# Kernel optimization log

Measured on AMD Instinct MI355X. Metric: run time of the kernel, lower is better.

## Reference

```python
import jax, jax.numpy as jnp
import numpy as np

NQ = 6; DM = 128; CH = 4; SEQ = 2048; CHUNK = 16; BATCH = 128
NFP = 5 * NQ * 2   # feature params for 2 layers
NMP = 5 * NQ * 2   # mixing params for 2 layers

# ---- batched gate matrices (theta: (B,)) ----

def _rx(t):
    c = jnp.cos(t / 2).astype(jnp.complex64)
    s = (-1j * jnp.sin(t / 2)).astype(jnp.complex64)
    return jnp.stack([jnp.stack([c, s], -1), jnp.stack([s, c], -1)], -2)

def _ry(t):
    c = jnp.cos(t / 2).astype(jnp.complex64)
    s = jnp.sin(t / 2).astype(jnp.complex64)
    return jnp.stack([jnp.stack([c, -s], -1), jnp.stack([s, c], -1)], -2)

def _rz(t):
    e = jnp.exp(-1j * t.astype(jnp.complex64) / 2)
    z = jnp.zeros_like(e)
    return jnp.stack([jnp.stack([e, z], -1), jnp.stack([z, jnp.conj(e)], -1)], -2)

def _crx(t):
    B = t.shape[0]
    r = _rx(t)
    I = jnp.broadcast_to(jnp.eye(2, dtype=jnp.complex64), (B, 2, 2))
    Z = jnp.zeros((B, 2, 2), jnp.complex64)
    return jnp.concatenate([jnp.concatenate([I, Z], -1), jnp.concatenate([Z, r], -1)], -2)

# ---- batched statevector gate application; state: (B, 2, ..., 2) with axis 1+w = wire w ----

def _ap1(s, U, w):
    s = jnp.moveaxis(s, 1 + w, 1)
    sh = s.shape
    s = jnp.einsum('bij,bjr->bir', U, s.reshape(sh[0], 2, -1)).reshape(sh)
    return jnp.moveaxis(s, 1, 1 + w)

def _ap2(s, U, w0, w1):
    s = jnp.moveaxis(s, (1 + w0, 1 + w1), (1, 2))
    sh = s.shape
    s = jnp.einsum('bij,bjr->bir', U, s.reshape(sh[0], 4, -1)).reshape(sh)
    return jnp.moveaxis(s, (1, 2), (1 + w0, 1 + w1))

def _ansatz(s, p, off):
    # RX,RY,RZ on each qubit, then forward CRX ring, then backward CRX ring
    for i in range(NQ):
        s = _ap1(s, _rx(p[:, off + 3 * i]), i)
        s = _ap1(s, _ry(p[:, off + 3 * i + 1]), i)
        s = _ap1(s, _rz(p[:, off + 3 * i + 2]), i)
    off += 3 * NQ
    for i in range(NQ):
        s = _ap2(s, _crx(p[:, off]), i, (i + 1) % NQ)
        off += 1
    for i in range(NQ - 1, -1, -1):
        s = _ap2(s, _crx(p[:, off]), i, (i - 1) % NQ)
        off += 1
    return s, off

def _circuit(angles, fp, mp):
    B = angles.shape[0]
    s = jnp.zeros((B, 2 ** NQ), jnp.complex64).at[:, 0].set(1.0).reshape((B,) + (2,) * NQ)
    for i in range(NQ):                      # RY input embedding
        s = _ap1(s, _ry(angles[:, i]), i)
    off = 0
    for _ in range(2):                        # feature layers
        s, off = _ansatz(s, fp, off)
    off = 0
    for _ in range(2):                        # mixing layers
        s, off = _ansatz(s, mp, off)
    xs, ys, zs = [], [], []
    for i in range(NQ):                       # <X_i>, <Y_i>, <Z_i>
        v = jnp.moveaxis(s, 1 + i, 1).reshape(B, 2, -1)
        a, b = v[:, 0], v[:, 1]
        ab = jnp.sum(jnp.conj(a) * b, -1)
        xs.append(2 * jnp.real(ab))
        ys.append(2 * jnp.imag(ab))
        zs.append(jnp.sum(jnp.abs(a) ** 2 - jnp.abs(b) ** 2, -1))
    return jnp.stack(xs + ys + zs, 1)         # (B, 18) ordered X..Y..Z

def _ln(x, g, b, eps=1e-5):
    m = x.mean(-1, keepdims=True)
    v = ((x - m) ** 2).mean(-1, keepdims=True)
    return (x - m) / jnp.sqrt(v + eps) * g + b

def _fwd(x, conv_w, conv_b, ln1_g, ln1_b, ca1_w, ca1_b, ca2_w, ca2_b, pp_w, pp_b,
         ep_w, ep_b, op_w, op_b, ln2_g, ln2_b, sa1_w, sa1_b, sa2_w, sa2_b,
         cl1_w, cl1_b, cl2_w, cl2_b):
    B, C, S = x.shape
    h = jax.lax.conv_general_dilated(x, conv_w, (1,), [(1, 1)],
                                     dimension_numbers=('NCH', 'OIH', 'NCH')) + conv_b[None, :, None]
    h = jnp.transpose(h, (0, 2, 1))           # (B, S, D)
    h = _ln(h, ln1_g, ln1_b)
    nchunks = S // CHUNK
    h = h.reshape(B * nchunks, CHUNK, DM)
    sc = jnp.tanh(h @ ca1_w + ca1_b) @ ca2_w + ca2_b
    w = jax.nn.softmax(sc, axis=1)
    summ = jnp.sum(w * h, axis=1)             # (B*nchunks, D)
    ap = summ @ pp_w + pp_b
    fp, mp = ap[:, :NFP], ap[:, NFP:]
    ang = jnp.tanh(summ @ ep_w + ep_b) * np.pi
    q = _circuit(ang, fp, mp)                 # (B*nchunks, 18)
    cf = jax.nn.silu(_ln(q @ op_w + op_b, ln2_g, ln2_b))  # dropout = eval identity
    cf = cf.reshape(B, nchunks, DM)
    ss = jnp.tanh(cf @ sa1_w + sa1_b) @ sa2_w + sa2_b
    sw = jax.nn.softmax(ss, axis=1)
    rep = jnp.sum(sw * cf, axis=1)
    return jax.nn.silu(rep @ cl1_w + cl1_b) @ cl2_w + cl2_b

def setup_inputs() -> dict:
    key = jax.random.key(0)
    ks = jax.random.split(key, 16)
    n = lambda k, sh: (jax.random.normal(k, sh, jnp.float32) * 0.05)
    return {
        'x': jax.random.normal(ks[0], (BATCH, CH, SEQ), jnp.float32),
        'conv_w': n(ks[1], (DM, CH, 3)), 'conv_b': jnp.zeros((DM,), jnp.float32),
        'ln1_g': jnp.ones((DM,), jnp.float32), 'ln1_b': jnp.zeros((DM,), jnp.float32),
        'ca1_w': n(ks[2], (DM, DM // 4)), 'ca1_b': jnp.zeros((DM // 4,), jnp.float32),
        'ca2_w': n(ks[3], (DM // 4, 1)), 'ca2_b': jnp.zeros((1,), jnp.float32),
        'pp_w': n(ks[4], (DM, NFP + NMP)), 'pp_b': jnp.zeros((NFP + NMP,), jnp.float32),
        'ep_w': n(ks[5], (DM, NQ)), 'ep_b': jnp.zeros((NQ,), jnp.float32),
        'op_w': n(ks[6], (3 * NQ, DM)), 'op_b': jnp.zeros((DM,), jnp.float32),
        'ln2_g': jnp.ones((DM,), jnp.float32), 'ln2_b': jnp.zeros((DM,), jnp.float32),
        'sa1_w': n(ks[7], (DM, DM // 4)), 'sa1_b': jnp.zeros((DM // 4,), jnp.float32),
        'sa2_w': n(ks[8], (DM // 4, 1)), 'sa2_b': jnp.zeros((1,), jnp.float32),
        'cl1_w': n(ks[9], (DM, DM // 2)), 'cl1_b': jnp.zeros((DM // 2,), jnp.float32),
        'cl2_w': n(ks[10], (DM // 2, 2)), 'cl2_b': jnp.zeros((2,), jnp.float32),
    }

def reference(x, conv_w, conv_b, ln1_g, ln1_b, ca1_w, ca1_b, ca2_w, ca2_b, pp_w, pp_b,
              ep_w, ep_b, op_w, op_b, ln2_g, ln2_b, sa1_w, sa1_b, sa2_w, sa2_b,
              cl1_w, cl1_b, cl2_w, cl2_b):
    return _fwd(x, conv_w, conv_b, ln1_g, ln1_b, ca1_w, ca1_b, ca2_w, ca2_b, pp_w, pp_b,
                ep_w, ep_b, op_w, op_b, ln2_g, ln2_b, sa1_w, sa1_b, sa2_w, sa2_b,
                cl1_w, cl1_b, cl2_w, cl2_b)
```

## Files before the change

kernel.cpp:

```cpp
#include <hip/hip_runtime.h>
#include <math.h>


constexpr int kNQ    = 6;
constexpr int kDM    = 128;
constexpr int kCH    = 4;
constexpr int kSEQ   = 2048;
constexpr int kCHUNK = 16;
constexpr int kBATCH = 128;
constexpr int kNCH   = kSEQ / kCHUNK;
constexpr int kNP    = 120;
constexpr float kPI  = 3.14159265358979323846f;

typedef __attribute__((ext_vector_type(8))) short bf16x8;
typedef __attribute__((ext_vector_type(4))) float f32x4;

__device__ __forceinline__ float fast_tanh(float x) {
  float e = __expf(-2.f * fabsf(x));
  float r = (1.f - e) * __builtin_amdgcn_rcpf(1.f + e);
  return copysignf(r, x);
}
__device__ __forceinline__ float fast_silu(float x) {
  return x * __builtin_amdgcn_rcpf(1.f + __expf(-x));
}
// ... 62 lines not shown
}

__device__ __forceinline__ void rz_lane(float c, float sp, float* sr, float* si) {
#pragma unroll
  for (int r = 0; r < 16; ++r) {
    float ar = sr[r], ai = si[r];
    sr[r] = fmaf(c, ar, -sp * ai);
    si[r] = fmaf(c, ai,  sp * ar);
  }
}

template <int RB, int CB>
__device__ __forceinline__ void crx_reg_reg(float c, float s, float* sr, float* si) {
#pragma unroll
  for (int r0 = 0; r0 < 16; ++r0) {
    if ((r0 & RB) || !(r0 & CB)) continue;
    int r1 = r0 | RB;
    float ar = sr[r0], ai = si[r0], br = sr[r1], bi = si[r1];
    sr[r0] = fmaf(c, ar,  s * bi);  si[r0] = fmaf(c, ai, -s * br);
    sr[r1] = fmaf(c, br,  s * ai);  si[r1] = fmaf(c, bi, -s * ar);
  }
}

template <int XM, int CB>
__device__ __forceinline__ void crx_reg_lane(float c, float s, float* sr, float* si) {
#pragma unroll
  for (int r = 0; r < 16; ++r) {
    if (!(r & CB)) continue;
    float pr = qp<XM>(sr[r]), pi = qp<XM>(si[r]);
    sr[r] = fmaf(c, sr[r],  s * pi);
    si[r] = fmaf(c, si[r], -s * pr);
  }
}

template <int RB>
__device__ __forceinline__ void meas_reg(const float* sr, const float* si,
                                         float& tr, float& ti, float& zz) {
  tr = 0.f; ti = 0.f; zz = 0.f;
#pragma unroll
  for (int r0 = 0; r0 < 16; ++r0) {
    float n = fmaf(sr[r0], sr[r0], si[r0] * si[r0]);
    zz += (r0 & RB) ? -n : n;
    if (r0 & RB) continue;
    int r1 = r0 | RB;
    tr = fmaf(sr[r0], sr[r1], fmaf(si[r0], si[r1], tr));
    ti = fmaf(sr[r0], si[r1], fmaf(-si[r0], sr[r1], ti));
  }
  tr += qp<1>(tr); tr += qp<2>(tr);
  ti += qp<1>(ti); ti += qp<2>(ti);
  zz += qp<1>(zz); zz += qp<2>(zz);
}


__global__ __launch_bounds__(128) void k_pre8(
    const float* __restrict__ x,
    const float* __restrict__ conv_w, const float* __restrict__ conv_b,
    const float* __restrict__ ln1_g,  const float* __restrict__ ln1_b,
    const float* __restrict__ ca1_w,  const float* __restrict__ ca1_b,
    const float* __restrict__ ca2_w,  const float* __restrict__ ca2_b,
    const float* __restrict__ pp_w,   const float* __restrict__ pp_b,
    const float* __restrict__ ep_w,   const float* __restrict__ ep_b,
    float* __restrict__ outb, int emit_cs)
{
  constexpr int NC = 8;

  __shared__ __align__(16) float xs[kCH][NC * kCHUNK + 4];
  __shared__ __align__(16) float hbuf[kCHUNK][132];
  __shared__ __align__(16) float spart[2][16];
  __shared__ __align__(16) float wl[kCHUNK];
  __shared__ __align__(16) float sums[NC][kDM];
  __shared__ float mrow[kCHUNK], irow[kCHUNK];

  const int tid    = threadIdx.x;
  const int chunk0 = blockIdx.x * NC;
  const int b      = chunk0 >> 7;
  const int tloc   = (chunk0 & 127) * kCHUNK;
  const int d      = tid;
  const int lane   = tid & 63;
  const int wv     = tid >> 6;
  const int col    = (lane & 15) + 16 * wv;
  const int qd     = lane >> 4;

  float w12[12];
  {
    const float4* cw = (const float4*)(conv_w + d * 12);
    float4 a0 = cw[0], a1 = cw[1], a2 = cw[2];
    w12[0]=a0.x; w12[1]=a0.y; w12[2]=a0.z; w12[3]=a0.w;
    w12[4]=a1.x; w12[5]=a1.y; w12[6]=a1.z; w12[7]=a1.w;
    w12[8]=a2.x; w12[9]=a2.y; w12[10]=a2.z; w12[11]=a2.w;
  }
  float cb = conv_b[d];
  float g1 = ln1_g[d], b1 = ln1_b[d];
  float cb1 = ca1_b[col], cw2 = ca2_w[col], cb2 = ca2_b[0];

  bf16x8 bhi[4], blo[4];
#pragma unroll
  for (int ks = 0; ks < 4; ++ks)
#pragma unroll
    for (int jj = 0; jj < 8; ++jj) {
      float bvf = ca1_w[(ks * 32 + qd * 8 + jj) * 32 + col];
      unsigned bb = __float_as_uint(bvf);
      bhi[ks][jj] = (short)(bb >> 16);
      float lf = bvf - __uint_as_float(bb & 0xffff0000u);
      blo[ks][jj] = (short)(__float_as_uint(lf) >> 16);
    }

#pragma unroll
  for (int ch = 0; ch < kCH; ++ch) {
#pragma unroll
    for (int base = 0; base < 2; ++base) {
      int pos = base * 128 + tid;
      if (pos < NC * kCHUNK + 2) {
        int s = tloc - 1 + pos;
        float v = 0.f;
        if (s >= 0 && s < kSEQ) v = x[((size_t)b * kCH + ch) * kSEQ + s];
        xs[ch][pos] = v;
      }
    }
  }
  __syncthreads();

  for (int c = 0; c < NC; ++c) {
    float h[kCHUNK];
#pragma unroll
    for (int t = 0; t < kCHUNK; ++t) h[t] = cb;
#pragma unroll
    for (int ch = 0; ch < kCH; ++ch) {
      const float4* xp = (const float4*)&xs[ch][c * kCHUNK];
      float4 v0 = xp[0], v1 = xp[1], v2 = xp[2], v3 = xp[3], v4 = xp[4];
      float xr[18];
      xr[0]=v0.x; xr[1]=v0.y; xr[2]=v0.z; xr[3]=v0.w;
      xr[4]=v1.x; xr[5]=v1.y; xr[6]=v1.z; xr[7]=v1.w;
      xr[8]=v2.x; xr[9]=v2.y; xr[10]=v2.z; xr[11]=v2.w;
      xr[12]=v3.x; xr[13]=v3.y; xr[14]=v3.z; xr[15]=v3.w;
      xr[16]=v4.x; xr[17]=v4.y;
      float c0 = w12[ch*3+0], c1 = w12[ch*3+1], c2 = w12[ch*3+2];
#pragma unroll
      for (int t = 0; t < kCHUNK; ++t)
        h[t] = fmaf(xr[t], c0, fmaf(xr[t+1], c1, fmaf(xr[t+2], c2, h[t])));
    }
#pragma unroll
    for (int t = 0; t < kCHUNK; ++t) hbuf[t][d] = h[t];
    __syncthreads();

    {
      int row = tid >> 3, k = tid & 7;
      const float4* rp = (const float4*)&hbuf[row][k * 16];
      float s1 = 0.f, s2 = 0.f;
#pragma unroll
      for (int q = 0; q < 4; ++q) {
        float4 v = rp[q];
        s1 += v.x + v.y + v.z + v.w;
        s2 = fmaf(v.x,v.x,s2); s2 = fmaf(v.y,v.y,s2);
        s2 = fmaf(v.z,v.z,s2); s2 = fmaf(v.w,v.w,s2);
      }
#pragma unroll
      for (int o = 1; o < 8; o <<= 1) {
        s1 += __shfl_xor(s1, o, 64);
        s2 += __shfl_xor(s2, o, 64);
      }
      if (k == 0) {
        float m = s1 * (1.f / kDM);
        mrow[row] = m;
        irow[row] = rsqrtf(s2 * (1.f / kDM) - m * m + 1e-5f);
      }
    }
    __syncthreads();

#pragma unroll
    for (int t = 0; t < kCHUNK; ++t) {
      h[t] = fmaf((h[t] - mrow[t]) * irow[t], g1, b1);
      unsigned hb = __float_as_uint(h[t]);
      float lof = h[t] - __uint_as_float(hb & 0xffff0000u);
      unsigned pk = (hb >> 16) | (__float_as_uint(lof) & 0xffff0000u);
      ((unsigned*)&hbuf[t][0])[d] = pk;
    }
    __syncthreads();

    f32x4 acc = {0.f, 0.f, 0.f, 0.f};
    {
      const unsigned* hrow = (const unsigned*)&hbuf[lane & 15][0];
#pragma unroll
      for (int ks = 0; ks < 4; ++ks) {
        const uint4* ap = (const uint4*)(hrow + ks * 32 + qd * 8);
        uint4 w0 = ap[0], w1 = ap[1];
        bf16x8 ahi, alo;
        ahi[0] = (short)(w0.x & 0xffff); ahi[1] = (short)(w0.y & 0xffff);
        ahi[2] = (short)(w0.z & 0xffff); ahi[3] = (short)(w0.w & 0xffff);
        ahi[4] = (short)(w1.x & 0xffff); ahi[5] = (short)(w1.y & 0xffff);
        ahi[6] = (short)(w1.z & 0xffff); ahi[7] = (short)(w1.w & 0xffff);
        alo[0] = (short)(w0.x >> 16); alo[1] = (short)(w0.y >> 16);
        alo[2] = (short)(w0.z >> 16); alo[3] = (short)(w0.w >> 16);
        alo[4] = (short)(w1.x >> 16); alo[5] = (short)(w1.y >> 16);
        alo[6] = (short)(w1.z >> 16); alo[7] = (short)(w1.w >> 16);
        acc = __builtin_amdgcn_mfma_f32_16x16x32_bf16(ahi, bhi[ks], acc, 0, 0, 0);
        acc = __builtin_amdgcn_mfma_f32_16x16x32_bf16(ahi, blo[ks], acc, 0, 0, 0);
        acc = __builtin_amdgcn_mfma_f32_16x16x32_bf16(alo, bhi[ks], acc, 0, 0, 0);
      }
    }

    {
      float ev[4];
#pragma unroll
      for (int r = 0; r < 4; ++r)
        ev[r] = fast_tanh(acc[r] + cb1) * cw2;
#pragma unroll
      for (int o = 1; o < 16; o <<= 1)
#pragma unroll
        for (int r = 0; r < 4; ++r) ev[r] += __shfl_xor(ev[r], o, 64);
      if ((lane & 15) == 0)
        *(float4*)&spart[wv][qd * 4] = make_float4(ev[0], ev[1], ev[2], ev[3]);
    }
    __syncthreads();

    if (tid < 16) {
      float scl = spart[0][tid] + spart[1][tid] + cb2;
      float mx = scl;
#pragma unroll
      for (int o = 1; o < 16; o <<= 1) mx = fmaxf(mx, __shfl_xor(mx, o, 64));
      float e = __expf(scl - mx);
      float se = e;
#pragma unroll
      for (int o = 1; o < 16; o <<= 1) se += __shfl_xor(se, o, 64);
      wl[tid] = e * (1.f / se);
    }
    __syncthreads();

    {
      const float4* w4 = (const float4*)wl;
      float4 wa = w4[0], wb = w4[1], wc = w4[2], wd = w4[3];
      float acc2 = 0.f;
      acc2 = fmaf(wa.x, h[0],  acc2); acc2 = fmaf(wa.y, h[1],  acc2);
      acc2 = fmaf(wa.z, h[2],  acc2); acc2 = fmaf(wa.w, h[3],  acc2);
      acc2 = fmaf(wb.x, h[4],  acc2); acc2 = fmaf(wb.y, h[5],  acc2);
      acc2 = fmaf(wb.z, h[6],  acc2); acc2 = fmaf(wb.w, h[7],  acc2);
      acc2 = fmaf(wc.x, h[8],  acc2); acc2 = fmaf(wc.y, h[9],  acc2);
      acc2 = fmaf(wc.z, h[10], acc2); acc2 = fmaf(wc.w, h[11], acc2);
      acc2 = fmaf(wd.x, h[12], acc2); acc2 = fmaf(wd.y, h[13], acc2);
      acc2 = fmaf(wd.z, h[14], acc2); acc2 = fmaf(wd.w, h[15], acc2);
      sums[c][d] = acc2;
    }
  }
  __syncthreads();

  if (tid < kNP + kNQ) {
    const bool isep = (tid >= kNP);
    const int  jj   = tid - kNP;
    const float* wp = isep ? (ep_w + jj) : (pp_w + tid);
    const int  ws   = isep ? kNQ : kNP;
    const int  ws2  = ws * 2, ws3 = ws * 3, ws4 = ws * 4;
    float bias = isep ? ep_b[jj] : pp_b[tid];
    float accp[NC];
#pragma unroll
    for (int c = 0; c < NC; ++c) accp[c] = bias;
#pragma unroll 4
    for (int q4 = 0; q4 < 32; ++q4) {
      float w0 = wp[0], w1 = wp[ws], w2 = wp[ws2], w3 = wp[ws3];
      wp += ws4;
#pragma unroll
      for (int c = 0; c < NC; ++c) {
        float4 s = *(const float4*)&sums[c][q4 * 4];
        accp[c] = fmaf(s.x, w0, fmaf(s.y, w1, fmaf(s.z, w2, fmaf(s.w, w3, accp[c]))));
      }
    }
    const int slot = isep ? jj : (6 + tid);
#pragma unroll
    for (int c = 0; c < NC; ++c) {
      int chunkg = chunk0 + c;
      float ha = isep ? (0.5f * fast_tanh(accp[c]) * kPI) : (0.5f * accp[c]);
      if (emit_cs) {
        ((float2*)(outb + (size_t)chunkg * 256))[slot] =
            make_float2(__cosf(ha), __sinf(ha));
      } else {
        outb[(size_t)chunkg * 126 + slot] = ha;
      }
    }
  }
}


constexpr int kCsStride = 260;

__global__ __launch_bounds__(64) void k_circ_cs(const float* __restrict__ csA,
                                                float* __restrict__ qv_g)
{
  __shared__ __align__(16) float lds[16 * kCsStride];

  const int lane  = threadIdx.x;
  const int c     = lane >> 2;
  const int l     = lane & 3;
  const int chunk = blockIdx.x * 16 + c;
  const int b0 = (l >> 1) & 1;
  const int b1 = l & 1;

  {
    const float4* src = (const float4*)(csA + (size_t)blockIdx.x * 16 * 256);
#pragma unroll
    for (int i = 0; i < 16; ++i) {
      float4 v = src[i * 64 + lane];
      *(float4*)&lds[i * kCsStride + lane * 4] = v;
    }
  }
  __syncthreads();

  const float2* cp = (const float2*)&lds[c * kCsStride];

  float sr[16], si[16];
#pragma unroll
  for (int r = 0; r < 16; ++r) { sr[r] = 0.f; si[r] = 0.f; }
  sr[0] = (l == 0) ? 1.f : 0.f;

  {
    float2 q0 = cp[0], q1 = cp[1], q2 = cp[2], q3 = cp[3], q4 = cp[4], q5 = cp[5];
    ry_lane<2>(q0.x, b0 ? q0.y : -q0.y, sr, si);
    ry_lane<1>(q1.x, b1 ? q1.y : -q1.y, sr, si);
    ry_reg<8>(q2.x, q2.y, sr, si);
    ry_reg<4>(q3.x, q3.y, sr, si);
    ry_reg<2>(q4.x, q4.y, sr, si);
    ry_reg<1>(q5.x, q5.y, sr, si);
  }

  for (int a = 0; a < 4; ++a) {
    const float2* pb = cp + 6 + a * 30;
    float2 t;
    t = pb[0];  rx_lane<2>(t.x, t.y, sr, si);
    t = pb[1];  ry_lane<2>(t.x, b0 ? t.y : -t.y, sr, si);
    t = pb[2];  rz_lane   (t.x, b0 ? t.y : -t.y, sr, si);
    t = pb[3];  rx_lane<1>(t.x, t.y, sr, si);
    t = pb[4];  ry_lane<1>(t.x, b1 ? t.y : -t.y, sr, si);
    t = pb[5];  rz_lane   (t.x, b1 ? t.y : -t.y, sr, si);
    t = pb[6];  rx_reg<8>(t.x, t.y, sr, si);
    t = pb[7];  ry_reg<8>(t.x, t.y, sr, si);
    t = pb[8];  rz_reg<8>(t.x, t.y, sr, si);
    t = pb[9];  rx_reg<4>(t.x, t.y, sr, si);
    t = pb[10]; ry_reg<4>(t.x, t.y, sr, si);
    t = pb[11]; rz_reg<4>(t.x, t.y, sr, si);
    t = pb[12]; rx_reg<2>(t.x, t.y, sr, si);
    t = pb[13]; ry_reg<2>(t.x, t.y, sr, si);
    t = pb[14]; rz_reg<2>(t.x, t.y, sr, si);
    t = pb[15]; rx_reg<1>(t.x, t.y, sr, si);
    t = pb[16]; ry_reg<1>(t.x, t.y, sr, si);
    t = pb[17]; rz_reg<1>(t.x, t.y, sr, si);
    t = pb[18]; { float c2 = b0 ? t.x : 1.f, s2 = b0 ? t.y : 0.f; rx_lane<1>(c2, s2, sr, si); }
    t = pb[19]; { float c2 = b1 ? t.x : 1.f, s2 = b1 ? t.y : 0.f; rx_reg<8>(c2, s2, sr, si); }
    t = pb[20]; crx_reg_reg<4, 8>(t.x, t.y, sr, si);
    t = pb[21]; crx_reg_reg<2, 4>(t.x, t.y, sr, si);
    t = pb[22]; crx_reg_reg<1, 2>(t.x, t.y, sr, si);
    t = pb[23]; crx_reg_lane<2, 1>(t.x, t.y, sr, si);
    t = pb[24]; crx_reg_reg<2, 1>(t.x, t.y, sr, si);
    t = pb[25]; crx_reg_reg<4, 2>(t.x, t.y, sr, si);
    t = pb[26]; crx_reg_reg<8, 4>(t.x, t.y, sr, si);
    t = pb[27]; crx_reg_lane<1, 8>(t.x, t.y, sr, si);
    t = pb[28]; { float c2 = b1 ? t.x : 1.f, s2 = b1 ? t.y : 0.f; rx_lane<2>(c2, s2, sr, si); }
    t = pb[29]; { float c2 = b0 ? t.x : 1.f, s2 = b0 ? t.y : 0.f; rx_reg<1>(c2, s2, sr, si); }
  }

  float res[18];
  {
    float tr = 0.f, ti = 0.f, zz = 0.f;
#pragma unroll
    for (int r = 0; r < 16; ++r) {
      float pr = qp<2>(sr[r]), pi = qp<2>(si[r]);
      tr = fmaf(sr[r], pr, fmaf(si[r], pi, tr));
      ti = fmaf(sr[r], pi, fmaf(-si[r], pr, ti));
      zz = fmaf(sr[r], sr[r], fmaf(si[r], si[r], zz));
    }
    tr = b0 ? 0.f : tr;  ti = b0 ? 0.f : ti;  zz = b0 ? -zz : zz;
    tr += qp<1>(tr); tr += qp<2>(tr);
    ti += qp<1>(ti); ti += qp<2>(ti);
    zz += qp<1>(zz); zz += qp<2>(zz);
    res[0] = 2.f * tr; res[6] = 2.f * ti; res[12] = zz;
  }
  {
    float tr = 0.f, ti = 0.f, zz = 0.f;
#pragma unroll
    for (int r = 0; r < 16; ++r) {
      float pr = qp<1>(sr[r]), pi = qp<1>(si[r]);
      tr = fmaf(sr[r], pr, fmaf(si[r], pi, tr));
      ti = fmaf(sr[r], pi, fmaf(-si[r], pr, ti));
      zz = fmaf(sr[r], sr[r], fmaf(si[r], si[r], zz));
    }
    tr = b1 ? 0.f : tr;  ti = b1 ? 0.f : ti;  zz = b1 ? -zz : zz;
    tr += qp<1>(tr); tr += qp<2>(tr);
    ti += qp<1>(ti); ti += qp<2>(ti);
    zz += qp<1>(zz); zz += qp<2>(zz);
    res[1] = 2.f * tr; res[7] = 2.f * ti; res[13] = zz;
  }
  {
    float tr, ti, zz;
    meas_reg<8>(sr, si, tr, ti, zz); res[2] = 2.f*tr; res[8]  = 2.f*ti; res[14] = zz;
    meas_reg<4>(sr, si, tr, ti, zz); res[3] = 2.f*tr; res[9]  = 2.f*ti; res[15] = zz;
    meas_reg<2>(sr, si, tr, ti, zz); res[4] = 2.f*tr; res[10] = 2.f*ti; res[16] = zz;
    meas_reg<1>(sr, si, tr, ti, zz); res[5] = 2.f*tr; res[11] = 2.f*ti; res[17] = zz;
  }
  if (l == 0) {
    float* qo = qv_g + (size_t)chunk * 18;
#pragma unroll
    for (int k = 0; k < 18; ++k) qo[k] = res[k];
  }
}


__global__ __launch_bounds__(64) void k_circ(const float* __restrict__ csb_g,
                                             float* __restrict__ qv_g)
{
  const int lane  = threadIdx.x;
  const int c     = lane >> 2;
  const int l     = lane & 3;
  const int chunk = blockIdx.x * 16 + c;
  const float* cp = csb_g + (size_t)chunk * 126;
  const int b0 = (l >> 1) & 1;
  const int b1 = l & 1;

  float sr[16], si[16];
#pragma unroll
  for (int r = 0; r < 16; ++r) { sr[r] = 0.f; si[r] = 0.f; }
  sr[0] = (l == 0) ? 1.f : 0.f;

  {
    float gc[6], gs[6];
#pragma unroll
    for (int g = 0; g < 6; ++g) { float th = cp[g]; gc[g] = __cosf(th); gs[g] = __sinf(th); }
    ry_lane<2>(gc[0], b0 ? gs[0] : -gs[0], sr, si);
    ry_lane<1>(gc[1], b1 ? gs[1] : -gs[1], sr, si);
    ry_reg<8>(gc[2], gs[2], sr, si);
    ry_reg<4>(gc[3], gs[3], sr, si);
    ry_reg<2>(gc[4], gs[4], sr, si);
    ry_reg<1>(gc[5], gs[5], sr, si);
  }

  for (int a = 0; a < 4; ++a) {
    const float* pb = cp + 6 + a * 30;
    float gc[30], gs[30];
#pragma unroll
    for (int g = 0; g < 30; ++g) { float th = pb[g]; gc[g] = __cosf(th); gs[g] = __sinf(th); }
    rx_lane<2>(gc[0], gs[0], sr, si);
    ry_lane<2>(gc[1], b0 ? gs[1] : -gs[1], sr, si);
    rz_lane   (gc[2], b0 ? gs[2] : -gs[2], sr, si);
    rx_lane<1>(gc[3], gs[3], sr, si);
    ry_lane<1>(gc[4], b1 ? gs[4] : -gs[4], sr, si);
    rz_lane   (gc[5], b1 ? gs[5] : -gs[5], sr, si);
    rx_reg<8>(gc[6],  gs[6],  sr, si);  ry_reg<8>(gc[7],  gs[7],  sr, si);  rz_reg<8>(gc[8],  gs[8],  sr, si);
    rx_reg<4>(gc[9],  gs[9],  sr, si);  ry_reg<4>(gc[10], gs[10], sr, si);  rz_reg<4>(gc[11], gs[11], sr, si);
    rx_reg<2>(gc[12], gs[12], sr, si);  ry_reg<2>(gc[13], gs[13], sr, si);  rz_reg<2>(gc[14], gs[14], sr, si);
    rx_reg<1>(gc[15], gs[15], sr, si);  ry_reg<1>(gc[16], gs[16], sr, si);  rz_reg<1>(gc[17], gs[17], sr, si);
    { float c2 = b0 ? gc[18] : 1.f, s2 = b0 ? gs[18] : 0.f; rx_lane<1>(c2, s2, sr, si); }
    { float c2 = b1 ? gc[19] : 1.f, s2 = b1 ? gs[19] : 0.f; rx_reg<8>(c2, s2, sr, si); }
// ... 434 lines not shown
  int tid = threadIdx.x, wid = tid >> 6, lane = tid & 63;
  int pair = blockIdx.x * 4 + wid;
  int j = lane & 31, hh = lane >> 5;
  const float4* row = (const float4*)(cf + (size_t)pair*kDM + hh*64);
  const float* wp = sa1_w + (hh*64)*32 + j;
  float acc = 0.f;
#pragma unroll
  for (int q = 0; q < 16; ++q) {
    float4 v = row[q];
    acc = fmaf(v.x,wp[(q*4+0)*32],acc); acc = fmaf(v.y,wp[(q*4+1)*32],acc);
    acc = fmaf(v.z,wp[(q*4+2)*32],acc); acc = fmaf(v.w,wp[(q*4+3)*32],acc);
  }
  acc += __shfl_xor(acc, 32, 64);
  float hv = fast_tanh(acc + sa1_b[j]);
  float v = hv * sa2_w[j];
#pragma unroll
  for (int o = 16; o; o >>= 1) v += __shfl_xor(v, o, 64);
  if (lane == 0) scl[pair] = v + sa2_b[0];
}


extern "C" void kernel_launch(void* const* d_in, const int* in_sizes, int n_in,
                              void* d_out, int out_size, void* d_ws, size_t ws_size,
                              hipStream_t stream) {
  const float* x      = (const float*)d_in[0];
  const float* conv_w = (const float*)d_in[1];
  const float* conv_b = (const float*)d_in[2];
  const float* ln1_g  = (const float*)d_in[3];
  const float* ln1_b  = (const float*)d_in[4];
  const float* ca1_w  = (const float*)d_in[5];
  const float* ca1_b  = (const float*)d_in[6];
  const float* ca2_w  = (const float*)d_in[7];
  const float* ca2_b  = (const float*)d_in[8];
  const float* pp_w   = (const float*)d_in[9];
  const float* pp_b   = (const float*)d_in[10];
  const float* ep_w   = (const float*)d_in[11];
  const float* ep_b   = (const float*)d_in[12];
  const float* op_w   = (const float*)d_in[13];
  const float* op_b   = (const float*)d_in[14];
  const float* ln2_g  = (const float*)d_in[15];
  const float* ln2_b  = (const float*)d_in[16];
  const float* sa1_w  = (const float*)d_in[17];
  const float* sa1_b  = (const float*)d_in[18];
  const float* sa2_w  = (const float*)d_in[19];
  const float* sa2_b  = (const float*)d_in[20];
  const float* cl1_w  = (const float*)d_in[21];
  const float* cl1_b  = (const float*)d_in[22];
  const float* cl2_w  = (const float*)d_in[23];
  const float* cl2_b  = (const float*)d_in[24];
  float* out = (float*)d_out;

  const size_t nch   = (size_t)kBATCH * kNCH;
  const size_t fCS   = nch * 256;
  const size_t need1 = (fCS + nch * 18 + nch) * sizeof(float);
  const size_t fA    = nch * kDM;
  const size_t need2 = (fA + nch * 18 + nch) * sizeof(float);

  if (ws_size >= need1) {
    float* csA   = (float*)d_ws;
    float* cf    = csA;
    float* qv_g  = csA + fCS;
    float* sclb  = qv_g + nch * 18;
    k_pre8<<<(kBATCH * kNCH) / 8, 128, 0, stream>>>(
        x, conv_w, conv_b, ln1_g, ln1_b, ca1_w, ca1_b, ca2_w, ca2_b,
        pp_w, pp_b, ep_w, ep_b, csA, 1);
    k_circ_cs<<<(kBATCH * kNCH) / 16, 64, 0, stream>>>(csA, qv_g);
    k_post<<<kBATCH * kNCH, 128, 0, stream>>>(
        qv_g, op_w, op_b, ln2_g, ln2_b, sa1_w, sa1_b, sa2_w, sa2_b, cf, sclb);
    k_pool_cf<<<kBATCH, 512, 0, stream>>>(
        cf, sclb, cl1_w, cl1_b, cl2_w, cl2_b, out);
  } else if (ws_size >= need2) {
    float* A     = (float*)d_ws;
    float* qv_g  = A + fA;
    float* sclb  = qv_g + nch * 18;
    k_pre8<<<(kBATCH * kNCH) / 8, 128, 0, stream>>>(
        x, conv_w, conv_b, ln1_g, ln1_b, ca1_w, ca1_b, ca2_w, ca2_b,
        pp_w, pp_b, ep_w, ep_b, A, 0);
    k_circ<<<(kBATCH * kNCH) / 16, 64, 0, stream>>>(A, qv_g);
    k_post<<<kBATCH * kNCH, 128, 0, stream>>>(
        qv_g, op_w, op_b, ln2_g, ln2_b, sa1_w, sa1_b, sa2_w, sa2_b, A, sclb);
    k_pool_cf<<<kBATCH, 512, 0, stream>>>(
        A, sclb, cl1_w, cl1_b, cl2_w, cl2_b, out);
  } else {
    float* cf   = (float*)d_ws;
    float* sclb = cf + nch * kDM;
    k_chunk_fb<<<kBATCH * kNCH, 128, 0, stream>>>(
        x, conv_w, conv_b, ln1_g, ln1_b, ca1_w, ca1_b, ca2_w, ca2_b,
        pp_w, pp_b, ep_w, ep_b, op_w, op_b, ln2_g, ln2_b, cf);
    k_scl_fb<<<(kBATCH * kNCH) / 4, 256, 0, stream>>>(cf, sa1_w, sa1_b, sa2_w, sa2_b, sclb);
    k_pool_cf<<<kBATCH, 512, 0, stream>>>(cf, sclb, cl1_w, cl1_b, cl2_w, cl2_b, out);
  }
}
```

Measured before the change: 208.2 us.

## Fuse quantum circuit simulation with post-processing into one kernel

Adds a k_circ_post64 kernel that simulates the circuit for 64 chunks per block and then, in the same block, applies the output projection, LayerNorm, SiLU and the attention scoring. The circuit simulation is moved into a shared device helper. This removes the separate k_circ_cs and k_post launches and the global round trip of the 18 measurement values per chunk. When the workspace is large enough, the new path replaces the old one and keeps cf in a separate buffer instead of overwriting csA. The cost is more LDS per block (about 90KB) and fewer, larger blocks, which lowers occupancy.

Result: faster. 200.9 us (-3.5%).

```diff
diff --git a/kernel.cpp b/kernel.cpp
--- a/kernel.cpp
+++ b/kernel.cpp
@@ -138,259 +138,9 @@
 }
 
 
-__global__ __launch_bounds__(128) void k_pre8(
-    const float* __restrict__ x,
-    const float* __restrict__ conv_w, const float* __restrict__ conv_b,
-    const float* __restrict__ ln1_g,  const float* __restrict__ ln1_b,
-    const float* __restrict__ ca1_w,  const float* __restrict__ ca1_b,
-    const float* __restrict__ ca2_w,  const float* __restrict__ ca2_b,
-    const float* __restrict__ pp_w,   const float* __restrict__ pp_b,
-    const float* __restrict__ ep_w,   const float* __restrict__ ep_b,
-    float* __restrict__ outb, int emit_cs)
-{
-  constexpr int NC = 8;
-
-  __shared__ __align__(16) float xs[kCH][NC * kCHUNK + 4];
-  __shared__ __align__(16) float hbuf[kCHUNK][132];
-  __shared__ __align__(16) float spart[2][16];
-  __shared__ __align__(16) float wl[kCHUNK];
-  __shared__ __align__(16) float sums[NC][kDM];
-  __shared__ float mrow[kCHUNK], irow[kCHUNK];
-
-  const int tid    = threadIdx.x;
-  const int chunk0 = blockIdx.x * NC;
-  const int b      = chunk0 >> 7;
-  const int tloc   = (chunk0 & 127) * kCHUNK;
-  const int d      = tid;
-  const int lane   = tid & 63;
-  const int wv     = tid >> 6;
-  const int col    = (lane & 15) + 16 * wv;
-  const int qd     = lane >> 4;
-
-  float w12[12];
-  {
-    const float4* cw = (const float4*)(conv_w + d * 12);
-    float4 a0 = cw[0], a1 = cw[1], a2 = cw[2];
-    w12[0]=a0.x; w12[1]=a0.y; w12[2]=a0.z; w12[3]=a0.w;
-    w12[4]=a1.x; w12[5]=a1.y; w12[6]=a1.z; w12[7]=a1.w;
-    w12[8]=a2.x; w12[9]=a2.y; w12[10]=a2.z; w12[11]=a2.w;
-  }
-  float cb = conv_b[d];
-  float g1 = ln1_g[d], b1 = ln1_b[d];
-  float cb1 = ca1_b[col], cw2 = ca2_w[col], cb2 = ca2_b[0];
-
-  bf16x8 bhi[4], blo[4];
-#pragma unroll
-  for (int ks = 0; ks < 4; ++ks)
-#pragma unroll
-    for (int jj = 0; jj < 8; ++jj) {
-      float bvf = ca1_w[(ks * 32 + qd * 8 + jj) * 32 + col];
-      unsigned bb = __float_as_uint(bvf);
-      bhi[ks][jj] = (short)(bb >> 16);
-      float lf = bvf - __uint_as_float(bb & 0xffff0000u);
-      blo[ks][jj] = (short)(__float_as_uint(lf) >> 16);
-    }
-
-#pragma unroll
-  for (int ch = 0; ch < kCH; ++ch) {
-#pragma unroll
-    for (int base = 0; base < 2; ++base) {
-      int pos = base * 128 + tid;
-      if (pos < NC * kCHUNK + 2) {
-        int s = tloc - 1 + pos;
-        float v = 0.f;
-        if (s >= 0 && s < kSEQ) v = x[((size_t)b * kCH + ch) * kSEQ + s];
-        xs[ch][pos] = v;
-      }
-    }
-  }
-  __syncthreads();
-
-  for (int c = 0; c < NC; ++c) {
-    float h[kCHUNK];
-#pragma unroll
-    for (int t = 0; t < kCHUNK; ++t) h[t] = cb;
-#pragma unroll
-    for (int ch = 0; ch < kCH; ++ch) {
-      const float4* xp = (const float4*)&xs[ch][c * kCHUNK];
-      float4 v0 = xp[0], v1 = xp[1], v2 = xp[2], v3 = xp[3], v4 = xp[4];
-      float xr[18];
-      xr[0]=v0.x; xr[1]=v0.y; xr[2]=v0.z; xr[3]=v0.w;
-      xr[4]=v1.x; xr[5]=v1.y; xr[6]=v1.z; xr[7]=v1.w;
-      xr[8]=v2.x; xr[9]=v2.y; xr[10]=v2.z; xr[11]=v2.w;
-      xr[12]=v3.x; xr[13]=v3.y; xr[14]=v3.z; xr[15]=v3.w;
-      xr[16]=v4.x; xr[17]=v4.y;
-      float c0 = w12[ch*3+0], c1 = w12[ch*3+1], c2 = w12[ch*3+2];
-#pragma unroll
-      for (int t = 0; t < kCHUNK; ++t)
-        h[t] = fmaf(xr[t], c0, fmaf(xr[t+1], c1, fmaf(xr[t+2], c2, h[t])));
-    }
-#pragma unroll
-    for (int t = 0; t < kCHUNK; ++t) hbuf[t][d] = h[t];
-    __syncthreads();
-
-    {
-      int row = tid >> 3, k = tid & 7;
-      const float4* rp = (const float4*)&hbuf[row][k * 16];
-      float s1 = 0.f, s2 = 0.f;
-#pragma unroll
-      for (int q = 0; q < 4; ++q) {
-        float4 v = rp[q];
-        s1 += v.x + v.y + v.z + v.w;
-        s2 = fmaf(v.x,v.x,s2); s2 = fmaf(v.y,v.y,s2);
-        s2 = fmaf(v.z,v.z,s2); s2 = fmaf(v.w,v.w,s2);
-      }
-#pragma unroll
-      for (int o = 1; o < 8; o <<= 1) {
-        s1 += __shfl_xor(s1, o, 64);
-        s2 += __shfl_xor(s2, o, 64);
-      }
-      if (k == 0) {
-        float m = s1 * (1.f / kDM);
-        mrow[row] = m;
-        irow[row] = rsqrtf(s2 * (1.f / kDM) - m * m + 1e-5f);
-      }
-    }
-    __syncthreads();
-
-#pragma unroll
-    for (int t = 0; t < kCHUNK; ++t) {
-      h[t] = fmaf((h[t] - mrow[t]) * irow[t], g1, b1);
-      unsigned hb = __float_as_uint(h[t]);
-      float lof = h[t] - __uint_as_float(hb & 0xffff0000u);
-      unsigned pk = (hb >> 16) | (__float_as_uint(lof) & 0xffff0000u);
-      ((unsigned*)&hbuf[t][0])[d] = pk;
-    }
-    __syncthreads();
-
-    f32x4 acc = {0.f, 0.f, 0.f, 0.f};
-    {
-      const unsigned* hrow = (const unsigned*)&hbuf[lane & 15][0];
-#pragma unroll
-      for (int ks = 0; ks < 4; ++ks) {
-        const uint4* ap = (const uint4*)(hrow + ks * 32 + qd * 8);
-        uint4 w0 = ap[0], w1 = ap[1];
-        bf16x8 ahi, alo;
-        ahi[0] = (short)(w0.x & 0xffff); ahi[1] = (short)(w0.y & 0xffff);
-        ahi[2] = (short)(w0.z & 0xffff); ahi[3] = (short)(w0.w & 0xffff);
-        ahi[4] = (short)(w1.x & 0xffff); ahi[5] = (short)(w1.y & 0xffff);
-        ahi[6] = (short)(w1.z & 0xffff); ahi[7] = (short)(w1.w & 0xffff);
-        alo[0] = (short)(w0.x >> 16); alo[1] = (short)(w0.y >> 16);
-        alo[2] = (short)(w0.z >> 16); alo[3] = (short)(w0.w >> 16);
-        alo[4] = (short)(w1.x >> 16); alo[5] = (short)(w1.y >> 16);
-        alo[6] = (short)(w1.z >> 16); alo[7] = (short)(w1.w >> 16);
-        acc = __builtin_amdgcn_mfma_f32_16x16x32_bf16(ahi, bhi[ks], acc, 0, 0, 0);
-        acc = __builtin_amdgcn_mfma_f32_16x16x32_bf16(ahi, blo[ks], acc, 0, 0, 0);
-        acc = __builtin_amdgcn_mfma_f32_16x16x32_bf16(alo, bhi[ks], acc, 0, 0, 0);
-      }
-    }
-
-    {
-      float ev[4];
-#pragma unroll
-      for (int r = 0; r < 4; ++r)
-        ev[r] = fast_tanh(acc[r] + cb1) * cw2;
-#pragma unroll
-      for (int o = 1; o < 16; o <<= 1)
-#pragma unroll
-        for (int r = 0; r < 4; ++r) ev[r] += __shfl_xor(ev[r], o, 64);
-      if ((lane & 15) == 0)
-        *(float4*)&spart[wv][qd * 4] = make_float4(ev[0], ev[1], ev[2], ev[3]);
-    }
-    __syncthreads();
-
-    if (tid < 16) {
-      float scl = spart[0][tid] + spart[1][tid] + cb2;
-      float mx = scl;
-#pragma unroll
-      for (int o = 1; o < 16; o <<= 1) mx = fmaxf(mx, __shfl_xor(mx, o, 64));
-      float e = __expf(scl - mx);
-      float se = e;
-#pragma unroll
-      for (int o = 1; o < 16; o <<= 1) se += __shfl_xor(se, o, 64);
-      wl[tid] = e * (1.f / se);
-    }
-    __syncthreads();
-
-    {
-      const float4* w4 = (const float4*)wl;
-      float4 wa = w4[0], wb = w4[1], wc = w4[2], wd = w4[3];
-      float acc2 = 0.f;
-      acc2 = fmaf(wa.x, h[0],  acc2); acc2 = fmaf(wa.y, h[1],  acc2);
-      acc2 = fmaf(wa.z, h[2],  acc2); acc2 = fmaf(wa.w, h[3],  acc2);
-      acc2 = fmaf(wb.x, h[4],  acc2); acc2 = fmaf(wb.y, h[5],  acc2);
-      acc2 = fmaf(wb.z, h[6],  acc2); acc2 = fmaf(wb.w, h[7],  acc2);
-      acc2 = fmaf(wc.x, h[8],  acc2); acc2 = fmaf(wc.y, h[9],  acc2);
-      acc2 = fmaf(wc.z, h[10], acc2); acc2 = fmaf(wc.w, h[11], acc2);
-      acc2 = fmaf(wd.x, h[12], acc2); acc2 = fmaf(wd.y, h[13], acc2);
-      acc2 = fmaf(wd.z, h[14], acc2); acc2 = fmaf(wd.w, h[15], acc2);
-      sums[c][d] = acc2;
-    }
-  }
-  __syncthreads();
-
-  if (tid < kNP + kNQ) {
-    const bool isep = (tid >= kNP);
-    const int  jj   = tid - kNP;
-    const float* wp = isep ? (ep_w + jj) : (pp_w + tid);
-    const int  ws   = isep ? kNQ : kNP;
-    const int  ws2  = ws * 2, ws3 = ws * 3, ws4 = ws * 4;
-    float bias = isep ? ep_b[jj] : pp_b[tid];
-    float accp[NC];
-#pragma unroll
-    for (int c = 0; c < NC; ++c) accp[c] = bias;
-#pragma unroll 4
-    for (int q4 = 0; q4 < 32; ++q4) {
-      float w0 = wp[0], w1 = wp[ws], w2 = wp[ws2], w3 = wp[ws3];
-      wp += ws4;
-#pragma unroll
-      for (int c = 0; c < NC; ++c) {
-        float4 s = *(const float4*)&sums[c][q4 * 4];
-        accp[c] = fmaf(s.x, w0, fmaf(s.y, w1, fmaf(s.z, w2, fmaf(s.w, w3, accp[c]))));
-      }
-    }
-    const int slot = isep ? jj : (6 + tid);
-#pragma unroll
-    for (int c = 0; c < NC; ++c) {
-      int chunkg = chunk0 + c;
-      float ha = isep ? (0.5f * fast_tanh(accp[c]) * kPI) : (0.5f * accp[c]);
-      if (emit_cs) {
-        ((float2*)(outb + (size_t)chunkg * 256))[slot] =
-            make_float2(__cosf(ha), __sinf(ha));
-      } else {
-        outb[(size_t)chunkg * 126 + slot] = ha;
-      }
-    }
-  }
-}
-
-
-constexpr int kCsStride = 260;
-
-__global__ __launch_bounds__(64) void k_circ_cs(const float* __restrict__ csA,
-                                                float* __restrict__ qv_g)
-{
-  __shared__ __align__(16) float lds[16 * kCsStride];
-
-  const int lane  = threadIdx.x;
-  const int c     = lane >> 2;
-  const int l     = lane & 3;
-  const int chunk = blockIdx.x * 16 + c;
-  const int b0 = (l >> 1) & 1;
-  const int b1 = l & 1;
-
-  {
-    const float4* src = (const float4*)(csA + (size_t)blockIdx.x * 16 * 256);
-#pragma unroll
-    for (int i = 0; i < 16; ++i) {
-      float4 v = src[i * 64 + lane];
-      *(float4*)&lds[i * kCsStride + lane * 4] = v;
-    }
-  }
-  __syncthreads();
-
-  const float2* cp = (const float2*)&lds[c * kCsStride];
-
+__device__ __forceinline__ void circ_from_cs(const float2* __restrict__ cp,
+                                             int l, int b0, int b1,
+                                             float* __restrict__ res) {
   float sr[16], si[16];
 #pragma unroll
   for (int r = 0; r < 16; ++r) { sr[r] = 0.f; si[r] = 0.f; }
@@ -441,7 +191,6 @@
     t = pb[29]; { float c2 = b0 ? t.x : 1.f, s2 = b0 ? t.y : 0.f; rx_reg<1>(c2, s2, sr, si); }
   }
 
-  float res[18];
   {
     float tr = 0.f, ti = 0.f, zz = 0.f;
 #pragma unroll
@@ -479,6 +228,372 @@
     meas_reg<2>(sr, si, tr, ti, zz); res[4] = 2.f*tr; res[10] = 2.f*ti; res[16] = zz;
     meas_reg<1>(sr, si, tr, ti, zz); res[5] = 2.f*tr; res[11] = 2.f*ti; res[17] = zz;
   }
+}
+
+
+__global__ __launch_bounds__(128) void k_pre8(
+    const float* __restrict__ x,
+    const float* __restrict__ conv_w, const float* __restrict__ conv_b,
+    const float* __restrict__ ln1_g,  const float* __restrict__ ln1_b,
+    const float* __restrict__ ca1_w,  const float* __restrict__ ca1_b,
+    const float* __restrict__ ca2_w,  const float* __restrict__ ca2_b,
+    const float* __restrict__ pp_w,   const float* __restrict__ pp_b,
+    const float* __restrict__ ep_w,   const float* __restrict__ ep_b,
+    float* __restrict__ outb, int emit_cs)
+{
+  constexpr int NC = 8;
+
+  __shared__ __align__(16) float xs[kCH][NC * kCHUNK + 4];
+  __shared__ __align__(16) float hbuf[kCHUNK][132];
+  __shared__ __align__(16) float spart[2][16];
+  __shared__ __align__(16) float wl[kCHUNK];
+  __shared__ __align__(16) float sums[NC][kDM];
+  __shared__ float mrow[kCHUNK], irow[kCHUNK];
+
+  const int tid    = threadIdx.x;
+  const int chunk0 = blockIdx.x * NC;
+  const int b      = chunk0 >> 7;
+  const int tloc   = (chunk0 & 127) * kCHUNK;
+  const int d      = tid;
+  const int lane   = tid & 63;
+  const int wv     = tid >> 6;
+  const int col    = (lane & 15) + 16 * wv;
+  const int qd     = lane >> 4;
+
+  float w12[12];
+  {
+    const float4* cw = (const float4*)(conv_w + d * 12);
+    float4 a0 = cw[0], a1 = cw[1], a2 = cw[2];
+    w12[0]=a0.x; w12[1]=a0.y; w12[2]=a0.z; w12[3]=a0.w;
+    w12[4]=a1.x; w12[5]=a1.y; w12[6]=a1.z; w12[7]=a1.w;
+    w12[8]=a2.x; w12[9]=a2.y; w12[10]=a2.z; w12[11]=a2.w;
+  }
+  float cb = conv_b[d];
+  float g1 = ln1_g[d], b1 = ln1_b[d];
+  float cb1 = ca1_b[col], cw2 = ca2_w[col], cb2 = ca2_b[0];
+
+  bf16x8 bhi[4], blo[4];
+#pragma unroll
+  for (int ks = 0; ks < 4; ++ks)
+#pragma unroll
+    for (int jj = 0; jj < 8; ++jj) {
+      float bvf = ca1_w[(ks * 32 + qd * 8 + jj) * 32 + col];
+      unsigned bb = __float_as_uint(bvf);
+      bhi[ks][jj] = (short)(bb >> 16);
+      float lf = bvf - __uint_as_float(bb & 0xffff0000u);
+      blo[ks][jj] = (short)(__float_as_uint(lf) >> 16);
+    }
+
+#pragma unroll
+  for (int ch = 0; ch < kCH; ++ch) {
+#pragma unroll
+    for (int base = 0; base < 2; ++base) {
+      int pos = base * 128 + tid;
+      if (pos < NC * kCHUNK + 2) {
+        int s = tloc - 1 + pos;
+        float v = 0.f;
+        if (s >= 0 && s < kSEQ) v = x[((size_t)b * kCH + ch) * kSEQ + s];
+        xs[ch][pos] = v;
+      }
+    }
+  }
+  __syncthreads();
+
+  for (int c = 0; c < NC; ++c) {
+    float h[kCHUNK];
+#pragma unroll
+    for (int t = 0; t < kCHUNK; ++t) h[t] = cb;
+#pragma unroll
+    for (int ch = 0; ch < kCH; ++ch) {
+      const float4* xp = (const float4*)&xs[ch][c * kCHUNK];
+      float4 v0 = xp[0], v1 = xp[1], v2 = xp[2], v3 = xp[3], v4 = xp[4];
+      float xr[18];
+      xr[0]=v0.x; xr[1]=v0.y; xr[2]=v0.z; xr[3]=v0.w;
+      xr[4]=v1.x; xr[5]=v1.y; xr[6]=v1.z; xr[7]=v1.w;
+      xr[8]=v2.x; xr[9]=v2.y; xr[10]=v2.z; xr[11]=v2.w;
+      xr[12]=v3.x; xr[13]=v3.y; xr[14]=v3.z; xr[15]=v3.w;
+      xr[16]=v4.x; xr[17]=v4.y;
+      float c0 = w12[ch*3+0], c1 = w12[ch*3+1], c2 = w12[ch*3+2];
+#pragma unroll
+      for (int t = 0; t < kCHUNK; ++t)
+        h[t] = fmaf(xr[t], c0, fmaf(xr[t+1], c1, fmaf(xr[t+2], c2, h[t])));
+    }
+#pragma unroll
+    for (int t = 0; t < kCHUNK; ++t) hbuf[t][d] = h[t];
+    __syncthreads();
+
+    {
+      int row = tid >> 3, k = tid & 7;
+      const float4* rp = (const float4*)&hbuf[row][k * 16];
+      float s1 = 0.f, s2 = 0.f;
+#pragma unroll
+      for (int q = 0; q < 4; ++q) {
+        float4 v = rp[q];
+        s1 += v.x + v.y + v.z + v.w;
+        s2 = fmaf(v.x,v.x,s2); s2 = fmaf(v.y,v.y,s2);
+        s2 = fmaf(v.z,v.z,s2); s2 = fmaf(v.w,v.w,s2);
+      }
+#pragma unroll
+      for (int o = 1; o < 8; o <<= 1) {
+        s1 += __shfl_xor(s1, o, 64);
+        s2 += __shfl_xor(s2, o, 64);
+      }
+      if (k == 0) {
+        float m = s1 * (1.f / kDM);
+        mrow[row] = m;
+        irow[row] = rsqrtf(s2 * (1.f / kDM) - m * m + 1e-5f);
+      }
+    }
+    __syncthreads();
+
+#pragma unroll
+    for (int t = 0; t < kCHUNK; ++t) {
+      h[t] = fmaf((h[t] - mrow[t]) * irow[t], g1, b1);
+      unsigned hb = __float_as_uint(h[t]);
+      float lof = h[t] - __uint_as_float(hb & 0xffff0000u);
+      unsigned pk = (hb >> 16) | (__float_as_uint(lof) & 0xffff0000u);
+      ((unsigned*)&hbuf[t][0])[d] = pk;
+    }
+    __syncthreads();
+
+    f32x4 acc = {0.f, 0.f, 0.f, 0.f};
+    {
+      const unsigned* hrow = (const unsigned*)&hbuf[lane & 15][0];
+#pragma unroll
+      for (int ks = 0; ks < 4; ++ks) {
+        const uint4* ap = (const uint4*)(hrow + ks * 32 + qd * 8);
+        uint4 w0 = ap[0], w1 = ap[1];
+        bf16x8 ahi, alo;
+        ahi[0] = (short)(w0.x & 0xffff); ahi[1] = (short)(w0.y & 0xffff);
+        ahi[2] = (short)(w0.z & 0xffff); ahi[3] = (short)(w0.w & 0xffff);
+        ahi[4] = (short)(w1.x & 0xffff); ahi[5] = (short)(w1.y & 0xffff);
+        ahi[6] = (short)(w1.z & 0xffff); ahi[7] = (short)(w1.w & 0xffff);
+        alo[0] = (short)(w0.x >> 16); alo[1] = (short)(w0.y >> 16);
+        alo[2] = (short)(w0.z >> 16); alo[3] = (short)(w0.w >> 16);
+        alo[4] = (short)(w1.x >> 16); alo[5] = (short)(w1.y >> 16);
+        alo[6] = (short)(w1.z >> 16); alo[7] = (short)(w1.w >> 16);
+        acc = __builtin_amdgcn_mfma_f32_16x16x32_bf16(ahi, bhi[ks], acc, 0, 0, 0);
+        acc = __builtin_amdgcn_mfma_f32_16x16x32_bf16(ahi, blo[ks], acc, 0, 0, 0);
+        acc = __builtin_amdgcn_mfma_f32_16x16x32_bf16(alo, bhi[ks], acc, 0, 0, 0);
+      }
+    }
+
+    {
+      float ev[4];
+#pragma unroll
+      for (int r = 0; r < 4; ++r)
+        ev[r] = fast_tanh(acc[r] + cb1) * cw2;
+#pragma unroll
+      for (int o = 1; o < 16; o <<= 1)
+#pragma unroll
+        for (int r = 0; r < 4; ++r) ev[r] += __shfl_xor(ev[r], o, 64);
+      if ((lane & 15) == 0)
+        *(float4*)&spart[wv][qd * 4] = make_float4(ev[0], ev[1], ev[2], ev[3]);
+    }
+    __syncthreads();
+
+    if (tid < 16) {
+      float scl = spart[0][tid] + spart[1][tid] + cb2;
+      float mx = scl;
+#pragma unroll
+      for (int o = 1; o < 16; o <<= 1) mx = fmaxf(mx, __shfl_xor(mx, o, 64));
+      float e = __expf(scl - mx);
+      float se = e;
+#pragma unroll
+      for (int o = 1; o < 16; o <<= 1) se += __shfl_xor(se, o, 64);
+      wl[tid] = e * (1.f / se);
+    }
+    __syncthreads();
+
+    {
+      const float4* w4 = (const float4*)wl;
+      float4 wa = w4[0], wb = w4[1], wc = w4[2], wd = w4[3];
+      float acc2 = 0.f;
+      acc2 = fmaf(wa.x, h[0],  acc2); acc2 = fmaf(wa.y, h[1],  acc2);
+      acc2 = fmaf(wa.z, h[2],  acc2); acc2 = fmaf(wa.w, h[3],  acc2);
+      acc2 = fmaf(wb.x, h[4],  acc2); acc2 = fmaf(wb.y, h[5],  acc2);
+      acc2 = fmaf(wb.z, h[6],  acc2); acc2 = fmaf(wb.w, h[7],  acc2);
+      acc2 = fmaf(wc.x, h[8],  acc2); acc2 = fmaf(wc.y, h[9],  acc2);
+      acc2 = fmaf(wc.z, h[10], acc2); acc2 = fmaf(wc.w, h[11], acc2);
+      acc2 = fmaf(wd.x, h[12], acc2); acc2 = fmaf(wd.y, h[13], acc2);
+      acc2 = fmaf(wd.z, h[14], acc2); acc2 = fmaf(wd.w, h[15], acc2);
+      sums[c][d] = acc2;
+    }
+  }
+  __syncthreads();
+
+  if (tid < kNP + kNQ) {
+    const bool isep = (tid >= kNP);
+    const int  jj   = tid - kNP;
+    const float* wp = isep ? (ep_w + jj) : (pp_w + tid);
+    const int  ws   = isep ? kNQ : kNP;
+    const int  ws2  = ws * 2, ws3 = ws * 3, ws4 = ws * 4;
+    float bias = isep ? ep_b[jj] : pp_b[tid];
+    float accp[NC];
+#pragma unroll
+    for (int c = 0; c < NC; ++c) accp[c] = bias;
+#pragma unroll 4
+    for (int q4 = 0; q4 < 32; ++q4) {
+      float w0 = wp[0], w1 = wp[ws], w2 = wp[ws2], w3 = wp[ws3];
+      wp += ws4;
+#pragma unroll
+      for (int c = 0; c < NC; ++c) {
+        float4 s = *(const float4*)&sums[c][q4 * 4];
+        accp[c] = fmaf(s.x, w0, fmaf(s.y, w1, fmaf(s.z, w2, fmaf(s.w, w3, accp[c]))));
+      }
+    }
+    const int slot = isep ? jj : (6 + tid);
+#pragma unroll
+    for (int c = 0; c < NC; ++c) {
+      int chunkg = chunk0 + c;
+      float ha = isep ? (0.5f * fast_tanh(accp[c]) * kPI) : (0.5f * accp[c]);
+      if (emit_cs) {
+        ((float2*)(outb + (size_t)chunkg * 256))[slot] =
+            make_float2(__cosf(ha), __sinf(ha));
+      } else {
+        outb[(size_t)chunkg * 126 + slot] = ha;
+      }
+    }
+  }
+}
+
+
+constexpr int kCsStride = 260;
+
+__global__ __launch_bounds__(256) void k_circ_post64(
+    const float* __restrict__ csA,
+    const float* __restrict__ op_w, const float* __restrict__ op_b,
+    const float* __restrict__ ln2_g, const float* __restrict__ ln2_b,
+    const float* __restrict__ sa1_w, const float* __restrict__ sa1_b,
+    const float* __restrict__ sa2_w, const float* __restrict__ sa2_b,
+    float* __restrict__ cf, float* __restrict__ sclb)
+{
+  __shared__ __align__(16) float lds[64 * kCsStride];
+  __shared__ __align__(16) float sa1s[128 * 32];
+  __shared__ __align__(16) float ops[18 * 128];
+  __shared__ __align__(16) float qvs[64][19];
+  __shared__ __align__(16) float cfw[4][128];
+
+  const int tid = threadIdx.x;
+  const int w   = tid >> 6;
+  const int l64 = tid & 63;
+
+  {
+    const float4* src = (const float4*)(csA +
+        ((size_t)blockIdx.x * 64 + w * 16) * 256);
+#pragma unroll
+    for (int i = 0; i < 16; ++i) {
+      float4 v = src[i * 64 + l64];
+      *(float4*)&lds[(w * 16 + i) * kCsStride + l64 * 4] = v;
+    }
+  }
+  {
+    const float4* s4 = (const float4*)sa1_w;
+    float4* d4 = (float4*)sa1s;
+#pragma unroll
+    for (int idx = tid; idx < 1024; idx += 256) d4[idx] = s4[idx];
+    const float4* o4 = (const float4*)op_w;
+    float4* p4 = (float4*)ops;
+#pragma unroll
+    for (int idx = tid; idx < 576; idx += 256) p4[idx] = o4[idx];
+  }
+  __syncthreads();
+
+  {
+    const int cl = w * 16 + (l64 >> 2);
+    const int l  = l64 & 3;
+    const int b0 = (l >> 1) & 1;
+    const int b1 = l & 1;
+    float res[18];
+    circ_from_cs((const float2*)&lds[cl * kCsStride], l, b0, b1, res);
+    if (l == 0) {
+#pragma unroll
+      for (int k = 0; k < 18; ++k) qvs[cl][k] = res[k];
+    }
+  }
+
+  const int j    = l64 & 31;
+  const int half = l64 >> 5;
+  const int d0   = l64 * 2;
+  float2 obv = *(const float2*)&op_b[d0];
+  float2 g2v = *(const float2*)&ln2_g[d0];
+  float2 b2v = *(const float2*)&ln2_b[d0];
+  float s1bj = sa1_b[j], s2wj = sa2_w[j], s2b = sa2_b[0];
+
+  for (int i = 0; i < 16; ++i) {
+    const int cl = w * 16 + i;
+    const int cg = blockIdx.x * 64 + cl;
+
+    float a0 = obv.x, a1 = obv.y;
+#pragma unroll
+    for (int k = 0; k < 18; ++k) {
+      float qk = qvs[cl][k];
+      float2 ow = *(const float2*)&ops[k * 128 + d0];
+      a0 = fmaf(qk, ow.x, a0);
+      a1 = fmaf(qk, ow.y, a1);
+    }
+
+    float v = a0 + a1, v2 = fmaf(a0, a0, a1 * a1);
+#pragma unroll
+    for (int o = 32; o; o >>= 1) {
+      v += __shfl_xor(v, o, 64);
+      v2 += __shfl_xor(v2, o, 64);
+    }
+    float m   = v * (1.f / kDM);
+    float var = v2 * (1.f / kDM) - m * m;
+    float inv = rsqrtf(var + 1e-5f);
+    float cf0 = fast_silu(fmaf((a0 - m) * inv, g2v.x, b2v.x));
+    float cf1 = fast_silu(fmaf((a1 - m) * inv, g2v.y, b2v.y));
+    *(float2*)&cf[(size_t)cg * kDM + d0] = make_float2(cf0, cf1);
+    *(float2*)&cfw[w][d0] = make_float2(cf0, cf1);
+
+    float acc2 = 0.f;
+    {
+      const float* cfr = &cfw[w][half * 64];
+      const float* swr = &sa1s[(half * 64) * 32 + j];
+#pragma unroll
+      for (int r = 0; r < 64; r += 4) {
+        float4 cv = *(const float4*)&cfr[r];
+        acc2 = fmaf(cv.x, swr[(r + 0) * 32], acc2);
+        acc2 = fmaf(cv.y, swr[(r + 1) * 32], acc2);
+        acc2 = fmaf(cv.z, swr[(r + 2) * 32], acc2);
+        acc2 = fmaf(cv.w, swr[(r + 3) * 32], acc2);
+      }
+    }
+    acc2 += __shfl_xor(acc2, 32, 64);
+    float hv = fast_tanh(acc2 + s1bj) * s2wj;
+#pragma unroll
+    for (int o = 16; o; o >>= 1) hv += __shfl_xor(hv, o, 64);
+    if (l64 == 0) sclb[cg] = hv + s2b;
+  }
+}
+
+
+__global__ __launch_bounds__(64) void k_circ_cs(const float* __restrict__ csA,
+                                                float* __restrict__ qv_g)
+{
+  __shared__ __align__(16) float lds[16 * kCsStride];
+
+  const int lane  = threadIdx.x;
+  const int c     = lane >> 2;
+  const int l     = lane & 3;
+  const int chunk = blockIdx.x * 16 + c;
+  const int b0 = (l >> 1) & 1;
+  const int b1 = l & 1;
+
+  {
+    const float4* src = (const float4*)(csA + (size_t)blockIdx.x * 16 * 256);
+#pragma unroll
+    for (int i = 0; i < 16; ++i) {
+      float4 v = src[i * 64 + lane];
+      *(float4*)&lds[i * kCsStride + lane * 4] = v;
+    }
+  }
+  __syncthreads();
+
+  float res[18];
+  circ_from_cs((const float2*)&lds[c * kCsStride], l, b0, b1, res);
+
   if (l == 0) {
     float* qo = qv_g + (size_t)chunk * 18;
 #pragma unroll
@@ -1019,11 +1134,23 @@
 
   const size_t nch   = (size_t)kBATCH * kNCH;
   const size_t fCS   = nch * 256;
+  const size_t fA    = nch * kDM;
+  const size_t need0 = (fCS + fA + nch) * sizeof(float);
   const size_t need1 = (fCS + nch * 18 + nch) * sizeof(float);
-  const size_t fA    = nch * kDM;
   const size_t need2 = (fA + nch * 18 + nch) * sizeof(float);
 
-  if (ws_size >= need1) {
+  if (ws_size >= need0) {
+    float* csA   = (float*)d_ws;
+    float* cf2   = csA + fCS;
+    float* sclb  = cf2 + fA;
+    k_pre8<<<(kBATCH * kNCH) / 8, 128, 0, stream>>>(
+        x, conv_w, conv_b, ln1_g, ln1_b, ca1_w, ca1_b, ca2_w, ca2_b,
+        pp_w, pp_b, ep_w, ep_b, csA, 1);
+    k_circ_post64<<<(kBATCH * kNCH) / 64, 256, 0, stream>>>(
+        csA, op_w, op_b, ln2_g, ln2_b, sa1_w, sa1_b, sa2_w, sa2_b, cf2, sclb);
+    k_pool_cf<<<kBATCH, 512, 0, stream>>>(
+        cf2, sclb, cl1_w, cl1_b, cl2_w, cl2_b, out);
+  } else if (ws_size >= need1) {
     float* csA   = (float*)d_ws;
     float* cf    = csA;
     float* qv_g  = csA + fCS;
```
